# Optimization experiments

Measured on AMD Instinct MI355X. Metric: run time of the kernel, lower is better.

The kernel has to match this reference:

```python
import jax, jax.numpy as jnp
import numpy as np

B, S, D, H = 4, 2048, 1024, 16
HD = D // H
SCALE = np.sqrt(HD).astype(np.float32)


def setup_inputs() -> dict:
    key = jax.random.key(0)
    ks = jax.random.split(key, 6)
    std = 1.0 / np.sqrt(D)
    return {
        "query": jax.random.normal(ks[0], (B, S, D), jnp.float32),
        "key": jax.random.normal(ks[1], (B, S, D), jnp.float32),
        "value": jax.random.normal(ks[2], (B, S, D), jnp.float32),
        "Wq": jax.random.normal(ks[3], (D, D), jnp.float32) * std,
        "bq": jnp.zeros((D,), jnp.float32),
        "Wk": jax.random.normal(ks[4], (D, D), jnp.float32) * std,
        "bk": jnp.zeros((D,), jnp.float32),
        "Wv": jax.random.normal(ks[5], (D, D), jnp.float32) * std,
        "bv": jnp.zeros((D,), jnp.float32),
    }


def _split_heads(x):
    # [B,S,D] -> [B,H,S,HD]
    return x.reshape(B, S, H, HD).transpose(0, 2, 1, 3)


def reference(query, key, value, Wq, bq, Wk, bk, Wv, bv):
    q = _split_heads(query @ Wq.T + bq)
    k = _split_heads(key @ Wk.T + bk)
    v = _split_heads(value @ Wv.T + bv)
    scores = jnp.einsum("bhqd,bhkd->bhqk", q, k) / SCALE
    attn = jax.nn.softmax(scores, axis=-1)  # dropout=0 (eval)
    ctx = jnp.einsum("bhqk,bhkd->bhqd", attn, v)
    return ctx.transpose(0, 2, 1, 3).reshape(B, S, D)
```

## Files before the change

### kernel.cpp

```cpp
#include <hip/hip_runtime.h>
#include <hip/hip_bf16.h>

typedef __attribute__((ext_vector_type(8))) short bf16x8;
typedef __attribute__((ext_vector_type(4))) float f32x4;
typedef __attribute__((ext_vector_type(16))) float f32x16;

#define SEQ 2048
#define DMODEL 1024
#define NH 16
#define HD 64
#define BATCH 4
#define BHTOT 64
#define BS 8192
#define QKV_ELEMS 8388608

#define C2EXP 0.1803368801111244f

__device__ __forceinline__ ushort f2bf(float f) {
  union { float f; unsigned u; } v; v.f = f;
  unsigned r = (v.u + 0x7FFFu + ((v.u >> 16) & 1u)) >> 16;
  return (ushort)r;
}

__device__ __forceinline__ unsigned pkbf(float a, float b) {
  union { __hip_bfloat162 h; unsigned u; } cv;
  cv.h = __float22bfloat162_rn(make_float2(a, b));
  return cv.u;
}

#if __has_builtin(__builtin_amdgcn_exp2f)
#define EXP2F(x) __builtin_amdgcn_exp2f(x)
#else
#define EXP2F(x) exp2f(x)
#endif

#define GLD16(gp, lp)                                                        \
  __builtin_amdgcn_global_load_lds(                                          \
      (const __attribute__((address_space(1))) void*)(gp),                   \
      (__attribute__((address_space(3))) void*)(lp), 16, 0, 0)

__global__ __launch_bounds__(256) void convert_w(
    const float* __restrict__ w0, const float* __restrict__ w1,
    const float* __restrict__ w2, ushort* __restrict__ out) {
  const float* src = blockIdx.y == 0 ? w0 : (blockIdx.y == 1 ? w1 : w2);
  size_t e = ((size_t)blockIdx.x * 256 + threadIdx.x) * 4;
  float4 v = *(const float4*)(src + e);
  ushort4 o = { f2bf(v.x), f2bf(v.y), f2bf(v.z), f2bf(v.w) };
  *(ushort4*)(out + (size_t)blockIdx.y * 1048576 + e) = o;
}

__global__ __launch_bounds__(256) void convert_x(
    const float* __restrict__ x0, const float* __restrict__ x1,
    const float* __restrict__ x2, ushort* __restrict__ out) {
  const float* src = blockIdx.y == 0 ? x0 : (blockIdx.y == 1 ? x1 : x2);
  size_t e = ((size_t)blockIdx.x * 256 + threadIdx.x) * 4;
  float4 v = *(const float4*)(src + e);
  ushort4 o = { f2bf(v.x), f2bf(v.y), f2bf(v.z), f2bf(v.w) };
  *(ushort4*)(out + (size_t)blockIdx.y * (size_t)QKV_ELEMS + e) = o;
}

__global__ __launch_bounds__(256) void qkv_gemm_bf(
    const ushort* __restrict__ Xb, const ushort* __restrict__ Wb,
    const float* __restrict__ bq, const float* __restrict__ bk, const float* __restrict__ bv,
    ushort* __restrict__ qkv) {
  __shared__ ushort sA[128][32];
  __shared__ ushort sB[128][32];

  const int z = blockIdx.z;
  const ushort* A = Xb + (size_t)z * QKV_ELEMS;
  const ushort* W = Wb + (size_t)z * 1048576;
  const float* bias = z == 0 ? bq : (z == 1 ? bk : bv);
  ushort* out = qkv + (size_t)z * QKV_ELEMS;

  const int t = threadIdx.x;
  const int m0 = blockIdx.x * 128;
  const int n0 = blockIdx.y * 128;
  const int w = t >> 6, l = t & 63, lr = l & 15, lhi = l >> 4;
  const int wr = (w >> 1) * 64, wc = (w & 1) * 64;

  const int rl = l >> 2;
  const int scol = ((l & 3) * 8) ^ ((rl & 3) << 3);
  const int rcol = (lhi * 8) ^ ((lr & 3) << 3);

  f32x4 acc[4][4];
#pragma unroll
  for (int i = 0; i < 4; i++)
#pragma unroll
    for (int j = 0; j < 4; j++) acc[i][j] = (f32x4){0.f, 0.f, 0.f, 0.f};

  for (int k0 = 0; k0 < DMODEL; k0 += 32) {
#pragma unroll
    for (int i = 0; i < 2; i++) {
      int c = w * 2 + i;
      GLD16(A + (size_t)(m0 + c * 16 + rl) * DMODEL + k0 + scol, &sA[c * 16][0]);
      GLD16(W + (size_t)(n0 + c * 16 + rl) * DMODEL + k0 + scol, &sB[c * 16][0]);
    }
    __syncthreads();
    bf16x8 af[4], bfr[4];
#pragma unroll
    for (int mi = 0; mi < 4; mi++) af[mi] = *(const bf16x8*)(&sA[wr + mi * 16 + lr][rcol]);
#pragma unroll
    for (int ni = 0; ni < 4; ni++) bfr[ni] = *(const bf16x8*)(&sB[wc + ni * 16 + lr][rcol]);
#pragma unroll
    for (int mi = 0; mi < 4; mi++)
#pragma unroll
      for (int ni = 0; ni < 4; ni++)
        acc[mi][ni] = __builtin_amdgcn_mfma_f32_16x16x32_bf16(af[mi], bfr[ni], acc[mi][ni], 0, 0, 0);
    __syncthreads();
  }

#pragma unroll
  for (int mi = 0; mi < 4; mi++) {
#pragma unroll
    for (int ni = 0; ni < 4; ni++) {
      int col = n0 + wc + ni * 16 + lr;
      float bsv = bias[col];
      int h = col >> 6, hd = col & 63;
#pragma unroll
      for (int r = 0; r < 4; r++) {
        int row = m0 + wr + mi * 16 + lhi * 4 + r;
        int b = row >> 11, s = row & 2047;
        float vv = acc[mi][ni][r] + bsv;
        out[(((size_t)(b * NH + h)) * SEQ + s) * HD + hd] = f2bf(vv);
      }
    }
  }
}

__global__ __launch_bounds__(256) void qkv_gemm_f32(
    const float* __restrict__ x0, const float* __restrict__ x1, const float* __restrict__ x2,
    const ushort* __restrict__ Wb,
    const float* __restrict__ bq, const float* __restrict__ bk, const float* __restrict__ bv,
    ushort* __restrict__ qkv) {
  __shared__ ushort sA[128][40];
  __shared__ ushort sB[128][40];

  const int z = blockIdx.z;
  const float* X = z == 0 ? x0 : (z == 1 ? x1 : x2);
  const ushort* W = Wb + (size_t)z * 1048576;
  const float* bias = z == 0 ? bq : (z == 1 ? bk : bv);
  ushort* out = qkv + (size_t)z * QKV_ELEMS;

  const int t = threadIdx.x;
  const int m0 = blockIdx.x * 128;
  const int n0 = blockIdx.y * 128;
  const int w = t >> 6, l = t & 63, lr = l & 15, lhi = l >> 4;
  const int wr = (w >> 1) * 64, wc = (w & 1) * 64;

  f32x4 acc[4][4];
#pragma unroll
  for (int i = 0; i < 4; i++)
#pragma unroll
    for (int j = 0; j < 4; j++) acc[i][j] = (f32x4){0.f, 0.f, 0.f, 0.f};

  for (int k0 = 0; k0 < DMODEL; k0 += 32) {
#pragma unroll
    for (int i = 0; i < 4; i++) {
      int e = i * 256 + t;
      int row = e >> 3, col = (e & 7) * 4;
      float4 a = *(const float4*)(X + (size_t)(m0 + row) * DMODEL + k0 + col);
      ushort4 ab = { f2bf(a.x), f2bf(a.y), f2bf(a.z), f2bf(a.w) };
      *(ushort4*)(&sA[row][col]) = ab;
      ushort4 bb = *(const ushort4*)(W + (size_t)(n0 + row) * DMODEL + k0 + col);
      *(ushort4*)(&sB[row][col]) = bb;
    }
    __syncthreads();
    bf16x8 af[4], bfr[4];
#pragma unroll
    for (int mi = 0; mi < 4; mi++) af[mi] = *(const bf16x8*)(&sA[wr + mi * 16 + lr][lhi * 8]);
#pragma unroll
    for (int ni = 0; ni < 4; ni++) bfr[ni] = *(const bf16x8*)(&sB[wc + ni * 16 + lr][lhi * 8]);
#pragma unroll
    for (int mi = 0; mi < 4; mi++)
#pragma unroll
      for (int ni = 0; ni < 4; ni++)
        acc[mi][ni] = __builtin_amdgcn_mfma_f32_16x16x32_bf16(af[mi], bfr[ni], acc[mi][ni], 0, 0, 0);
    __syncthreads();
  }

#pragma unroll
  for (int mi = 0; mi < 4; mi++) {
#pragma unroll
    for (int ni = 0; ni < 4; ni++) {
      int col = n0 + wc + ni * 16 + lr;
      float bsv = bias[col];
      int h = col >> 6, hd = col & 63;
#pragma unroll
      for (int r = 0; r < 4; r++) {
        int row = m0 + wr + mi * 16 + lhi * 4 + r;
        int b = row >> 11, s = row & 2047;
        float vv = acc[mi][ni][r] + bsv;
        out[(((size_t)(b * NH + h)) * SEQ + s) * HD + hd] = f2bf(vv);
      }
    }
  }
}

__global__ __launch_bounds__(256) void attn_kernel(const ushort* __restrict__ qkv,
                                                   float* __restrict__ out) {
  __shared__ ushort Kt[2][64][72];
  __shared__ ushort Vt[2][64][72];

  const int rb = blockIdx.x;
  const int bid = (rb & 7) * 128 + (rb >> 3);
  const int bh = bid >> 4, qt = bid & 15;
  const int q0 = qt * 128;
  const int t = threadIdx.x, w = t >> 6, l = t & 63;
  const int lq = l & 31, hi = l >> 5, hi8 = hi * 8;

  const ushort* q = qkv;
  const ushort* k = qkv + QKV_ELEMS;
  const ushort* v = qkv + 2 * (size_t)QKV_ELEMS;
  const size_t base = (size_t)bh * SEQ * HD;

  const int krow = t >> 3, kcol = (t & 7) * 8;
  const int skv = t & 63;
  const int skvp = (skv & 51) | ((skv & 4) << 1) | ((skv & 8) >> 1);
  const int shb = (t >> 6) * 8;

  bf16x8 aq[4];
  {
    int qrow = q0 + w * 32 + lq;
#pragma unroll
    for (int ks = 0; ks < 4; ks++)
      aq[ks] = *(const bf16x8*)(q + base + (size_t)qrow * HD + ks * 16 + hi8);
  }

  float m2 = -1e30f, lsum = 0.f;
  f32x16 acc_o[2];
  acc_o[0] = (f32x16)(0.0f);
  acc_o[1] = (f32x16)(0.0f);

#pragma unroll
  for (int i = 0; i < 2; i++) {
    bf16x8 gk = *(const bf16x8*)(k + base + (size_t)(i * 32 + krow) * HD + kcol);
    *(bf16x8*)(&Kt[0][i * 32 + krow][kcol]) = gk;
    bf16x8 gv = *(const bf16x8*)(v + base + (size_t)skv * HD + shb + i * 32);
#pragma unroll
    for (int j = 0; j < 8; j++) Vt[0][shb + i * 32 + j][skvp] = ((ushort)gv[j]);
  }
  __syncthreads();

  for (int tile = 0; tile < SEQ / 64; tile++) {
    const int cur = tile & 1, nxt = cur ^ 1;
    const int kvn = ((tile + 1) & 31) * 64;

    bf16x8 gk[2], gv[2];
#pragma unroll
    for (int i = 0; i < 2; i++) {
      gk[i] = *(const bf16x8*)(k + base + (size_t)(kvn + i * 32 + krow) * HD + kcol);
      gv[i] = *(const bf16x8*)(v + base + (size_t)(kvn + skv) * HD + shb + i * 32);
    }

    f32x16 sc[2];
    sc[0] = (f32x16)(0.0f);
    sc[1] = (f32x16)(0.0f);
#pragma unroll
    for (int mt = 0; mt < 2; mt++)
#pragma unroll
      for (int ks = 0; ks < 4; ks++) {
        bf16x8 ak = *(const bf16x8*)(&Kt[cur][mt * 32 + lq][ks * 16 + hi8]);
        sc[mt] = __builtin_amdgcn_mfma_f32_32x32x16_bf16(ak, aq[ks], sc[mt], 0, 0, 0);
      }

    float tm = sc[0][0];
#pragma unroll
    for (int mt = 0; mt < 2; mt++)
#pragma unroll
      for (int r = 0; r < 16; r++) tm = fmaxf(tm, sc[mt][r]);
    tm *= C2EXP;
    tm = fmaxf(tm, __shfl_xor(tm, 32));
    if (__any(tm > m2 + 8.f)) {
      float mn = fmaxf(m2, tm);
      float alpha = EXP2F(m2 - mn);
      m2 = mn;
      lsum *= alpha;
#pragma unroll
      for (int r = 0; r < 16; r++) {
        int rowq = (r & 3) + 8 * (r >> 2) + 4 * hi;
        float ar = __shfl(alpha, (l & 32) | rowq);
        acc_o[0][r] *= ar;
        acc_o[1][r] *= ar;
      }
    }

    float rs = 0.f;
    unsigned c[2][8];
#pragma unroll
    for (int mt = 0; mt < 2; mt++)
#pragma unroll
      for (int i = 0; i < 8; i++) {
        float p0 = EXP2F(sc[mt][2 * i] * C2EXP - m2);
        float p1 = EXP2F(sc[mt][2 * i + 1] * C2EXP - m2);
        rs += p0 + p1;
        c[mt][i] = pkbf(p0, p1);
      }
    rs += __shfl_xor(rs, 32);
    lsum += rs;

#pragma unroll
    for (int s = 0; s < 4; s++) {
      union { unsigned u[4]; bf16x8 v8; } ap;
#pragma unroll
      for (int j = 0; j < 4; j++) ap.u[j] = c[s >> 1][(s & 1) * 4 + j];
#pragma unroll
      for (int nt = 0; nt < 2; nt++) {
        bf16x8 bv = *(const bf16x8*)(&Vt[cur][nt * 32 + lq][s * 16 + hi8]);
        acc_o[nt] = __builtin_amdgcn_mfma_f32_32x32x16_bf16(ap.v8, bv, acc_o[nt], 0, 0, 0);
      }
    }

#pragma unroll
    for (int i = 0; i < 2; i++) {
      *(bf16x8*)(&Kt[nxt][i * 32 + krow][kcol]) = gk[i];
#pragma unroll
      for (int j = 0; j < 8; j++) Vt[nxt][shb + i * 32 + j][skvp] = ((ushort)gv[i][j]);
    }
    __syncthreads();
  }

  const int b = bh >> 4, h = bh & 15;
  float inv = 1.f / lsum;
#pragma unroll
  for (int r = 0; r < 16; r++) {
    int rowq = (r & 3) + 8 * (r >> 2) + 4 * hi;
    float iv = __shfl(inv, (l & 32) | rowq);
    int s = q0 + w * 32 + rowq;
#pragma unroll
    for (int nt = 0; nt < 2; nt++)
      out[((size_t)(b * SEQ + s)) * DMODEL + h * HD + nt * 32 + lq] = acc_o[nt][r] * iv;
  }
}

extern "C" void kernel_launch(void* const* d_in, const int* in_sizes, int n_in,
                              void* d_out, int out_size, void* d_ws, size_t ws_size,
                              hipStream_t stream) {
  const float* query = (const float*)d_in[0];
  const float* key_  = (const float*)d_in[1];
  const float* value = (const float*)d_in[2];
  const float* Wq = (const float*)d_in[3];
  const float* bq = (const float*)d_in[4];
  const float* Wk = (const float*)d_in[5];
  const float* bk = (const float*)d_in[6];
  const float* Wv = (const float*)d_in[7];
  const float* bv = (const float*)d_in[8];

  ushort* Wb = (ushort*)d_ws;
  ushort* qkv = Wb + 3u * 1048576u;
  ushort* Xb = qkv + 3u * (size_t)QKV_ELEMS;
  const size_t need = (3u * 1048576u + 6u * (size_t)QKV_ELEMS) * 2u;

  convert_w<<<dim3(1024, 3), 256, 0, stream>>>(Wq, Wk, Wv, Wb);
  if (ws_size >= need) {
    convert_x<<<dim3(8192, 3), 256, 0, stream>>>(query, key_, value, Xb);
    qkv_gemm_bf<<<dim3(64, 8, 3), 256, 0, stream>>>(Xb, Wb, bq, bk, bv, qkv);
  } else {
    qkv_gemm_f32<<<dim3(64, 8, 3), 256, 0, stream>>>(query, key_, value, Wb, bq, bk, bv, qkv);
  }
  attn_kernel<<<dim3(BHTOT * (SEQ / 128)), 256, 0, stream>>>(qkv, (float*)d_out);
}
```

Before: 206.0 us.

## Pre-transpose V, use direct global-to-LDS loads with XOR swizzle, fold softmax scale into Q

```diff
diff --git a/kernel.cpp b/kernel.cpp
--- a/kernel.cpp
+++ b/kernel.cpp
@@ -70,6 +70,7 @@
   const ushort* A = Xb + (size_t)z * QKV_ELEMS;
   const ushort* W = Wb + (size_t)z * 1048576;
   const float* bias = z == 0 ? bq : (z == 1 ? bk : bv);
+  const float oscale = z == 0 ? C2EXP : 1.0f;
   ushort* out = qkv + (size_t)z * QKV_ELEMS;
 
   const int t = threadIdx.x;
@@ -120,7 +121,7 @@
       for (int r = 0; r < 4; r++) {
         int row = m0 + wr + mi * 16 + lhi * 4 + r;
         int b = row >> 11, s = row & 2047;
-        float vv = acc[mi][ni][r] + bsv;
+        float vv = (acc[mi][ni][r] + bsv) * oscale;
         out[(((size_t)(b * NH + h)) * SEQ + s) * HD + hd] = f2bf(vv);
       }
     }
@@ -139,6 +140,7 @@
   const float* X = z == 0 ? x0 : (z == 1 ? x1 : x2);
   const ushort* W = Wb + (size_t)z * 1048576;
   const float* bias = z == 0 ? bq : (z == 1 ? bk : bv);
+  const float oscale = z == 0 ? C2EXP : 1.0f;
   ushort* out = qkv + (size_t)z * QKV_ELEMS;
 
   const int t = threadIdx.x;
@@ -189,17 +191,44 @@
       for (int r = 0; r < 4; r++) {
         int row = m0 + wr + mi * 16 + lhi * 4 + r;
         int b = row >> 11, s = row & 2047;
-        float vv = acc[mi][ni][r] + bsv;
+        float vv = (acc[mi][ni][r] + bsv) * oscale;
         out[(((size_t)(b * NH + h)) * SEQ + s) * HD + hd] = f2bf(vv);
       }
     }
   }
 }
 
+__global__ __launch_bounds__(256) void transpose_v(const ushort* __restrict__ vsrc,
+                                                   ushort* __restrict__ vtg) {
+  __shared__ ushort T[64][72];
+  const int s0 = blockIdx.x * 64;
+  const int bh = blockIdx.y;
+  const int t = threadIdx.x;
+  const int r = t >> 2, c16 = (t & 3) * 16;
+
+  const ushort* src = vsrc + ((size_t)bh * SEQ + s0 + r) * HD + c16;
+  uint4 a = *(const uint4*)(src);
+  uint4 b = *(const uint4*)(src + 8);
+  *(uint4*)(&T[r][c16]) = a;
+  *(uint4*)(&T[r][c16 + 8]) = b;
+  __syncthreads();
+
+  ushort o[16];
+#pragma unroll
+  for (int jj = 0; jj < 16; jj++) {
+    int sj = (jj & 3) | ((jj & 4) << 1) | ((jj & 8) >> 1);
+    o[jj] = T[c16 + sj][r];
+  }
+  ushort* dst = vtg + ((size_t)bh * HD + r) * SEQ + s0 + c16;
+  *(uint4*)(dst) = *(uint4*)(&o[0]);
+  *(uint4*)(dst + 8) = *(uint4*)(&o[8]);
+}
+
 __global__ __launch_bounds__(256) void attn_kernel(const ushort* __restrict__ qkv,
+                                                   const ushort* __restrict__ vtg,
                                                    float* __restrict__ out) {
-  __shared__ ushort Kt[2][64][72];
-  __shared__ ushort Vt[2][64][72];
+  __shared__ ushort Kt[2][64][64];
+  __shared__ ushort Vt[2][64][64];
 
   const int rb = blockIdx.x;
   const int bid = (rb & 7) * 128 + (rb >> 3);
@@ -209,14 +238,19 @@
   const int lq = l & 31, hi = l >> 5, hi8 = hi * 8;
 
   const ushort* q = qkv;
-  const ushort* k = qkv + QKV_ELEMS;
-  const ushort* v = qkv + 2 * (size_t)QKV_ELEMS;
   const size_t base = (size_t)bh * SEQ * HD;
-
-  const int krow = t >> 3, kcol = (t & 7) * 8;
-  const int skv = t & 63;
-  const int skvp = (skv & 51) | ((skv & 4) << 1) | ((skv & 8) >> 1);
-  const int shb = (t >> 6) * 8;
+  const ushort* kb = qkv + QKV_ELEMS + base;
+  const ushort* vb = vtg + (size_t)bh * HD * SEQ;
+
+  int rrow[2], scol[2];
+#pragma unroll
+  for (int i = 0; i < 2; i++) {
+    int g = w * 2 + i;
+    int r = g * 8 + (l >> 3);
+    rrow[i] = r;
+    scol[i] = ((l & 7) * 8) ^ ((r & 7) << 3);
+  }
+  const int rx = (lq & 7) << 3;
 
   bf16x8 aq[4];
   {
@@ -233,11 +267,8 @@
 
 #pragma unroll
   for (int i = 0; i < 2; i++) {
-    bf16x8 gk = *(const bf16x8*)(k + base + (size_t)(i * 32 + krow) * HD + kcol);
-    *(bf16x8*)(&Kt[0][i * 32 + krow][kcol]) = gk;
-    bf16x8 gv = *(const bf16x8*)(v + base + (size_t)skv * HD + shb + i * 32);
-#pragma unroll
-    for (int j = 0; j < 8; j++) Vt[0][shb + i * 32 + j][skvp] = ((ushort)gv[j]);
+    GLD16(kb + (size_t)rrow[i] * HD + scol[i], &Kt[0][(w * 2 + i) * 8][0]);
+    GLD16(vb + (size_t)rrow[i] * SEQ + scol[i], &Vt[0][(w * 2 + i) * 8][0]);
   }
   __syncthreads();
 
@@ -245,11 +276,10 @@
     const int cur = tile & 1, nxt = cur ^ 1;
     const int kvn = ((tile + 1) & 31) * 64;
 
-    bf16x8 gk[2], gv[2];
 #pragma unroll
     for (int i = 0; i < 2; i++) {
-      gk[i] = *(const bf16x8*)(k + base + (size_t)(kvn + i * 32 + krow) * HD + kcol);
-      gv[i] = *(const bf16x8*)(v + base + (size_t)(kvn + skv) * HD + shb + i * 32);
+      GLD16(kb + (size_t)(kvn + rrow[i]) * HD + scol[i], &Kt[nxt][(w * 2 + i) * 8][0]);
+      GLD16(vb + (size_t)rrow[i] * SEQ + kvn + scol[i], &Vt[nxt][(w * 2 + i) * 8][0]);
     }
 
     f32x16 sc[2];
@@ -259,16 +289,15 @@
     for (int mt = 0; mt < 2; mt++)
 #pragma unroll
       for (int ks = 0; ks < 4; ks++) {
-        bf16x8 ak = *(const bf16x8*)(&Kt[cur][mt * 32 + lq][ks * 16 + hi8]);
+        bf16x8 ak = *(const bf16x8*)(&Kt[cur][mt * 32 + lq][(ks * 16 + hi8) ^ rx]);
         sc[mt] = __builtin_amdgcn_mfma_f32_32x32x16_bf16(ak, aq[ks], sc[mt], 0, 0, 0);
       }
 
-    float tm = sc[0][0];
-#pragma unroll
-    for (int mt = 0; mt < 2; mt++)
-#pragma unroll
-      for (int r = 0; r < 16; r++) tm = fmaxf(tm, sc[mt][r]);
-    tm *= C2EXP;
+    float tm = fmaxf(sc[0][0], sc[0][1]);
+#pragma unroll
+    for (int r = 2; r < 16; r += 2) tm = fmaxf(fmaxf(sc[0][r], sc[0][r + 1]), tm);
+#pragma unroll
+    for (int r = 0; r < 16; r += 2) tm = fmaxf(fmaxf(sc[1][r], sc[1][r + 1]), tm);
     tm = fmaxf(tm, __shfl_xor(tm, 32));
     if (__any(tm > m2 + 8.f)) {
       float mn = fmaxf(m2, tm);
@@ -285,37 +314,26 @@
     }
 
     float rs = 0.f;
-    unsigned c[2][8];
-#pragma unroll
-    for (int mt = 0; mt < 2; mt++)
-#pragma unroll
-      for (int i = 0; i < 8; i++) {
-        float p0 = EXP2F(sc[mt][2 * i] * C2EXP - m2);
-        float p1 = EXP2F(sc[mt][2 * i + 1] * C2EXP - m2);
+#pragma unroll
+    for (int s = 0; s < 4; s++) {
+      const int mt = s >> 1, e0 = (s & 1) * 8;
+      union { unsigned u[4]; bf16x8 v8; } ap;
+#pragma unroll
+      for (int j = 0; j < 4; j++) {
+        float p0 = EXP2F(sc[mt][e0 + 2 * j] - m2);
+        float p1 = EXP2F(sc[mt][e0 + 2 * j + 1] - m2);
         rs += p0 + p1;
-        c[mt][i] = pkbf(p0, p1);
-      }
+        ap.u[j] = pkbf(p0, p1);
+      }
+#pragma unroll
+      for (int nt = 0; nt < 2; nt++) {
+        bf16x8 bv = *(const bf16x8*)(&Vt[cur][nt * 32 + lq][(s * 16 + hi8) ^ rx]);
+        acc_o[nt] = __builtin_amdgcn_mfma_f32_32x32x16_bf16(ap.v8, bv, acc_o[nt], 0, 0, 0);
+      }
+    }
     rs += __shfl_xor(rs, 32);
     lsum += rs;
 
-#pragma unroll
-    for (int s = 0; s < 4; s++) {
-      union { unsigned u[4]; bf16x8 v8; } ap;
-#pragma unroll
-      for (int j = 0; j < 4; j++) ap.u[j] = c[s >> 1][(s & 1) * 4 + j];
-#pragma unroll
-      for (int nt = 0; nt < 2; nt++) {
-        bf16x8 bv = *(const bf16x8*)(&Vt[cur][nt * 32 + lq][s * 16 + hi8]);
-        acc_o[nt] = __builtin_amdgcn_mfma_f32_32x32x16_bf16(ap.v8, bv, acc_o[nt], 0, 0, 0);
-      }
-    }
-
-#pragma unroll
-    for (int i = 0; i < 2; i++) {
-      *(bf16x8*)(&Kt[nxt][i * 32 + krow][kcol]) = gk[i];
-#pragma unroll
-      for (int j = 0; j < 8; j++) Vt[nxt][shb + i * 32 + j][skvp] = ((ushort)gv[i][j]);
-    }
     __syncthreads();
   }
 
@@ -348,14 +366,17 @@
   ushort* Wb = (ushort*)d_ws;
   ushort* qkv = Wb + 3u * 1048576u;
   ushort* Xb = qkv + 3u * (size_t)QKV_ELEMS;
-  const size_t need = (3u * 1048576u + 6u * (size_t)QKV_ELEMS) * 2u;
+  ushort* Vtg = Xb;
+  const size_t need_bf = (3u * 1048576u + 6u * (size_t)QKV_ELEMS) * 2u;
+  const size_t need_f32 = (3u * 1048576u + 4u * (size_t)QKV_ELEMS) * 2u;
 
   convert_w<<<dim3(1024, 3), 256, 0, stream>>>(Wq, Wk, Wv, Wb);
-  if (ws_size >= need) {
+  if (ws_size >= need_bf) {
     convert_x<<<dim3(8192, 3), 256, 0, stream>>>(query, key_, value, Xb);
     qkv_gemm_bf<<<dim3(64, 8, 3), 256, 0, stream>>>(Xb, Wb, bq, bk, bv, qkv);
-  } else {
+  } else if (ws_size >= need_f32) {
     qkv_gemm_f32<<<dim3(64, 8, 3), 256, 0, stream>>>(query, key_, value, Wb, bq, bk, bv, qkv);
   }
-  attn_kernel<<<dim3(BHTOT * (SEQ / 128)), 256, 0, stream>>>(qkv, (float*)d_out);
-}
+  transpose_v<<<dim3(SEQ / 64, BHTOT), 256, 0, stream>>>(qkv + 2u * (size_t)QKV_ELEMS, Vtg);
+  attn_kernel<<<dim3(BHTOT * (SEQ / 128)), 256, 0, stream>>>(qkv, Vtg, (float*)d_out);
+}
```

New measurement: 220.8 us. +7.2%, slower.
